# Performance work log

Hardware: AMD Instinct MI355X
Metric: run time of the kernel (lower is better)

Reference implementation:

```python
import jax, jax.numpy as jnp
import numpy as np

N = 50000          # nodes
E = 1600000        # edges
F_IN = 128         # node_features
H = 256            # hidden_dim
A = 16             # action_dim
G = 64             # num graphs in batch


def _sage_conv(x, src, dst, Wl, bl, Wr, num_nodes):
    # PyG SAGEConv (aggr='mean'): out = lin_l(mean_{j in N(i)} x_j) + lin_r(x_i)
    msgs = x[src]                                              # [E, F] gather
    agg = jax.ops.segment_sum(msgs, dst, num_segments=num_nodes)
    cnt = jax.ops.segment_sum(jnp.ones((src.shape[0], 1), x.dtype), dst,
                              num_segments=num_nodes)
    mean = agg / jnp.maximum(cnt, 1.0)                         # [N, F]
    return mean @ Wl + bl + x @ Wr


def setup_inputs() -> dict:
    key = jax.random.key(0)
    ks = jax.random.split(key, 16)
    s = lambda k, sh: jax.random.normal(k, sh, dtype=jnp.float32) * (1.0 / np.sqrt(sh[0]))
    inp = {
        "x": jax.random.normal(ks[0], (N, F_IN), dtype=jnp.float32),
        "edge_index": jax.random.randint(ks[1], (2, E), 0, N, dtype=jnp.int32),
        "batch": jnp.sort(jax.random.randint(ks[2], (N,), 0, G, dtype=jnp.int32)),
        # SAGEConv 1
        "Wl1": s(ks[3], (F_IN, H)), "bl1": jnp.zeros((H,), jnp.float32), "Wr1": s(ks[4], (F_IN, H)),
        # SAGEConv 2
        "Wl2": s(ks[5], (H, H)), "bl2": jnp.zeros((H,), jnp.float32), "Wr2": s(ks[6], (H, H)),
        # actor MLP
        "Wa1": s(ks[7], (H, H)), "ba1": jnp.zeros((H,), jnp.float32),
        "Wa2": s(ks[8], (H, A)), "ba2": jnp.zeros((A,), jnp.float32),
        # critic MLP
        "Wc1": s(ks[9], (H, H)), "bc1": jnp.zeros((H,), jnp.float32),
        "Wc2": s(ks[10], (H, 1)), "bc2": jnp.zeros((1,), jnp.float32),
    }
    return inp


def reference(x, edge_index, batch, Wl1, bl1, Wr1, Wl2, bl2, Wr2,
              Wa1, ba1, Wa2, ba2, Wc1, bc1, Wc2, bc2):
    src, dst = edge_index[0], edge_index[1]
    h = jax.nn.relu(_sage_conv(x, src, dst, Wl1, bl1, Wr1, N))
    h = jax.nn.relu(_sage_conv(h, src, dst, Wl2, bl2, Wr2, N))
    # global_mean_pool over graph ids
    pooled = jax.ops.segment_sum(h, batch, num_segments=G)
    gcnt = jax.ops.segment_sum(jnp.ones((N, 1), h.dtype), batch, num_segments=G)
    g = pooled / jnp.maximum(gcnt, 1.0)                        # [G, H]
    mu = jax.nn.relu(g @ Wa1 + ba1) @ Wa2 + ba2                # [G, A]
    value = jax.nn.relu(g @ Wc1 + bc1) @ Wc2 + bc2             # [G, 1]
    return mu, value
```

## Files before the change

### kernel.cpp

```cpp
#include <hip/hip_runtime.h>
#include <hip/hip_bf16.h>
#include <hip/hip_fp8.h>

#define NN 50000
#define NE 1600000
#define FIN 128
#define HH 256
#define GG 64
#define AA 16
#define NB ((NN + 255) / 256)
#define NRANGE 8
#define RSZ (NN / NRANGE)

typedef __attribute__((ext_vector_type(8))) short short8;
typedef __attribute__((ext_vector_type(4))) float f32x4;
typedef __attribute__((ext_vector_type(4))) int   i32x4;
typedef __attribute__((ext_vector_type(4))) uint  u32x4;

static __device__ __forceinline__ ushort f2b(float f) {
    union { __hip_bfloat16 h; ushort u; } v; v.h = __float2bfloat16(f); return v.u;
}
static __device__ __forceinline__ float b2f_lo(uint a) {
    union { float f; uint u; } v; v.u = a << 16; return v.f;
}
template<int SEL>
static __device__ __forceinline__ float f8tof(uint u) {
#if __has_builtin(__builtin_amdgcn_cvt_f32_fp8)
    return __builtin_amdgcn_cvt_f32_fp8(u, SEL);
#else
    union { unsigned char c; __hip_fp8_e4m3 f; } v;
    v.c = (u >> (SEL * 8)) & 0xFF;
    return (float)v.f;
#endif
}
static __device__ __forceinline__ unsigned char ftof8(float f) {
    __hip_fp8_e4m3 v(f);
    return *reinterpret_cast<unsigned char*>(&v);
}

__global__ void k_prep(const float* __restrict__ x, ushort* __restrict__ xb,
                       unsigned char* __restrict__ xf8,
                       const float* __restrict__ Wl1, const float* __restrict__ Wr1,
                       ushort* __restrict__ Wt1,
                       const float* __restrict__ Wl2, const float* __restrict__ Wr2,
                       ushort* __restrict__ Wt2,
                       int* __restrict__ degi, float* __restrict__ gz) {
    int b = blockIdx.x, t = threadIdx.x;
    if (b < 6250) {
        int i = b * 256 + t;
        float4 v = reinterpret_cast<const float4*>(x)[i];
        ushort4 o; o.x = f2b(v.x); o.y = f2b(v.y); o.z = f2b(v.z); o.w = f2b(v.w);
        reinterpret_cast<ushort4*>(xb)[i] = o;
        uchar4 p; p.x = ftof8(v.x); p.y = ftof8(v.y); p.z = ftof8(v.z); p.w = ftof8(v.w);
        reinterpret_cast<uchar4*>(xf8)[i] = p;
    } else if (b < 6506) {
        int i = (b - 6250) * 256 + t;
        int n = i / 256, k = i % 256;
        float v = (k < 128) ? Wl1[k * HH + n] : Wr1[(k - 128) * HH + n];
        Wt1[i] = f2b(v);
    } else if (b < 7018) {
        int i = (b - 6506) * 256 + t;
        int n = i / 512, k = i % 512;
        float v = (k < 256) ? Wl2[k * HH + n] : Wr2[(k - 256) * HH + n];
        Wt2[i] = f2b(v);
    } else if (b < 7214) {
        int i = (b - 7018) * 256 + t;
        if (i < NN) degi[i] = 0;
    } else {
        int i = (b - 7214) * 256 + t;
        if (i < GG + GG * HH) gz[i] = 0.0f;
    }
}

__global__ void k_degi(const int* __restrict__ dst, int* __restrict__ degi) {
    int range = blockIdx.x & 7;
    int i = (blockIdx.x >> 3) * 256 + threadIdx.x;
    if (i >= NE / 4) return;
    i32x4 d = __builtin_nontemporal_load(reinterpret_cast<const i32x4*>(dst) + i);
    int lo = range * RSZ, hi = lo + RSZ;
    if (d.x >= lo && d.x < hi) atomicAdd(&degi[d.x], 1);
    if (d.y >= lo && d.y < hi) atomicAdd(&degi[d.y], 1);
    if (d.z >= lo && d.z < hi) atomicAdd(&degi[d.z], 1);
    if (d.w >= lo && d.w < hi) atomicAdd(&degi[d.w], 1);
}

__global__ void k_gdeg(const int* __restrict__ batch, float* __restrict__ gcnt) {
    __shared__ float h[GG];
    int t = threadIdx.x;
    if (t < GG) h[t] = 0.0f;
    __syncthreads();
    int i = blockIdx.x * 256 + t;
    if (i < NN) atomicAdd(&h[batch[i]], 1.0f);
    __syncthreads();
    if (t < GG && h[t] != 0.0f) atomicAdd(&gcnt[t], h[t]);
}

__global__ void k_scan1(const int* __restrict__ degi, int* __restrict__ blocksum) {
    __shared__ int s[256];
    int t = threadIdx.x, i = blockIdx.x * 256 + t;
    s[t] = i < NN ? degi[i] : 0;
    __syncthreads();
    for (int d = 128; d > 0; d >>= 1) { if (t < d) s[t] += s[t + d]; __syncthreads(); }
    if (t == 0) blocksum[blockIdx.x] = s[0];
}

__global__ void k_scan2(const int* __restrict__ blocksum, int* __restrict__ blockoff) {
    __shared__ int s[256];
    int t = threadIdx.x;
    int v = t < NB ? blocksum[t] : 0;
    s[t] = v; __syncthreads();
    for (int d = 1; d < 256; d <<= 1) {
        int x = t >= d ? s[t - d] : 0; __syncthreads();
        s[t] += x; __syncthreads();
    }
    if (t < NB) blockoff[t] = s[t] - v;
}

__global__ void k_scan3(const int* __restrict__ degi, const int* __restrict__ blockoff,
                        int* __restrict__ offsets, int* __restrict__ cursor) {
    __shared__ int s[256];
    int t = threadIdx.x, i = blockIdx.x * 256 + t;
    int v = i < NN ? degi[i] : 0;
    s[t] = v; __syncthreads();
    for (int d = 1; d < 256; d <<= 1) {
        int x = t >= d ? s[t - d] : 0; __syncthreads();
        s[t] += x; __syncthreads();
    }
    if (i < NN) {
        int off = blockoff[blockIdx.x] + s[t] - v;
        offsets[i] = off;
        cursor[i]  = off;
    }
    if (i == 0) offsets[NN] = NE;
}

__global__ void k_fill(const int* __restrict__ src, const int* __restrict__ dst,
                       int* __restrict__ cursor, int* __restrict__ csr_src) {
    int range = blockIdx.x & 7;
    int i = (blockIdx.x >> 3) * 256 + threadIdx.x;
    if (i >= NE / 4) return;
    i32x4 d = __builtin_nontemporal_load(reinterpret_cast<const i32x4*>(dst) + i);
    i32x4 s = __builtin_nontemporal_load(reinterpret_cast<const i32x4*>(src) + i);
    int lo = range * RSZ, hi = lo + RSZ;
    if (d.x >= lo && d.x < hi) csr_src[atomicAdd(&cursor[d.x], 1)] = s.x;
    if (d.y >= lo && d.y < hi) csr_src[atomicAdd(&cursor[d.y], 1)] = s.y;
    if (d.z >= lo && d.z < hi) csr_src[atomicAdd(&cursor[d.z], 1)] = s.z;
    if (d.w >= lo && d.w < hi) csr_src[atomicAdd(&cursor[d.w], 1)] = s.w;
}

template<int C>
__global__ void __launch_bounds__(256) k_gatherf8(
        const int* __restrict__ offsets, const int* __restrict__ csr_src,
        const unsigned char* __restrict__ feat, ushort* __restrict__ agg) {
    constexpr int V = C / 64;
    int wid = threadIdx.x >> 6, lane = threadIdx.x & 63;
    int node = blockIdx.x * 4 + wid;
    if (node >= NN) return;
    int o0 = offsets[node], o1 = offsets[node + 1];
    const unsigned char* fp = feat + lane * V;
    float acc[V];
#pragma unroll
    for (int i = 0; i < V; i++) acc[i] = 0.0f;

    int t = o0;
    for (; t + 3 < o1; t += 4) {
        int s0 = __builtin_nontemporal_load(csr_src + t);
        int s1 = __builtin_nontemporal_load(csr_src + t + 1);
        int s2 = __builtin_nontemporal_load(csr_src + t + 2);
        int s3 = __builtin_nontemporal_load(csr_src + t + 3);
        if constexpr (V == 2) {
            uint u0 = *(const ushort*)(fp + (size_t)s0 * C);
            uint u1 = *(const ushort*)(fp + (size_t)s1 * C);
            uint u2 = *(const ushort*)(fp + (size_t)s2 * C);
            uint u3 = *(const ushort*)(fp + (size_t)s3 * C);
            acc[0] += (f8tof<0>(u0) + f8tof<0>(u1)) + (f8tof<0>(u2) + f8tof<0>(u3));
            acc[1] += (f8tof<1>(u0) + f8tof<1>(u1)) + (f8tof<1>(u2) + f8tof<1>(u3));
        } else {
            uint u0 = *(const uint*)(fp + (size_t)s0 * C);
            uint u1 = *(const uint*)(fp + (size_t)s1 * C);
            uint u2 = *(const uint*)(fp + (size_t)s2 * C);
            uint u3 = *(const uint*)(fp + (size_t)s3 * C);
            acc[0] += (f8tof<0>(u0) + f8tof<0>(u1)) + (f8tof<0>(u2) + f8tof<0>(u3));
            acc[1] += (f8tof<1>(u0) + f8tof<1>(u1)) + (f8tof<1>(u2) + f8tof<1>(u3));
            acc[2] += (f8tof<2>(u0) + f8tof<2>(u1)) + (f8tof<2>(u2) + f8tof<2>(u3));
            acc[3] += (f8tof<3>(u0) + f8tof<3>(u1)) + (f8tof<3>(u2) + f8tof<3>(u3));
        }
    }
    for (; t < o1; ++t) {
        int s0 = __builtin_nontemporal_load(csr_src + t);
        if constexpr (V == 2) {
            uint u0 = *(const ushort*)(fp + (size_t)s0 * C);
            acc[0] += f8tof<0>(u0); acc[1] += f8tof<1>(u0);
        } else {
            uint u0 = *(const uint*)(fp + (size_t)s0 * C);
            acc[0] += f8tof<0>(u0); acc[1] += f8tof<1>(u0);
            acc[2] += f8tof<2>(u0); acc[3] += f8tof<3>(u0);
        }
    }

    int deg = o1 - o0;
    float r = __builtin_amdgcn_rcpf(deg > 1 ? (float)deg : 1.0f);
    if constexpr (V == 2) {
        uint o = (uint)f2b(acc[0] * r) | ((uint)f2b(acc[1] * r) << 16);
        *(uint*)(agg + (size_t)node * C + lane * 2) = o;
    } else {
        uint2 o;
        o.x = (uint)f2b(acc[0] * r) | ((uint)f2b(acc[1] * r) << 16);
        o.y = (uint)f2b(acc[2] * r) | ((uint)f2b(acc[3] * r) << 16);
        *(uint2*)(agg + (size_t)node * C + lane * 4) = o;
    }
}

template<int K>
__global__ void __launch_bounds__(256) k_sage_mfma(
        const ushort* __restrict__ agg, const ushort* __restrict__ xin,
        const ushort* __restrict__ Wt, const float* __restrict__ bias,
        ushort* __restrict__ outb, unsigned char* __restrict__ out8) {
    constexpr int KH = K / 2;
    constexpr int LDP = 40;
    __shared__ ushort As[128 * LDP];
    __shared__ ushort Bs[256 * LDP];

    const int tid  = threadIdx.x;
    const int lane = tid & 63;
    const int w    = tid >> 6;
    const int base = blockIdx.x * 128;
    const int r    = lane & 15;
    const int kh   = lane >> 4;
    const int wcol = w * 64;

    f32x4 acc[8][4];
#pragma unroll
    for (int m = 0; m < 8; m++)
#pragma unroll
        for (int n = 0; n < 4; n++) acc[m][n] = (f32x4){0.f, 0.f, 0.f, 0.f};

    const int frowA = tid >> 1;
    const int fqA   = tid & 1;
    const int frowB = tid >> 2;
    const int fqB   = tid & 3;
    int fnode = base + frowA; if (fnode >= NN) fnode = 0;

    for (int k0 = 0; k0 < K; k0 += 32) {
        __syncthreads();
        {
            const ushort* srcp = (k0 < KH)
                ? agg + (size_t)fnode * KH + k0 + fqA * 16
                : xin + (size_t)fnode * KH + (k0 - KH) + fqA * 16;
            u32x4 a0 = *(const u32x4*)srcp;
            u32x4 a1 = *(const u32x4*)(srcp + 8);
            *(u32x4*)(&As[frowA * LDP + fqA * 16])     = a0;
            *(u32x4*)(&As[frowA * LDP + fqA * 16 + 8]) = a1;
        }
#pragma unroll
        for (int s = 0; s < 4; s++) {
            int c = frowB + s * 64;
            *(u32x4*)(&Bs[c * LDP + fqB * 8]) =
                *(const u32x4*)(Wt + (size_t)c * K + k0 + fqB * 8);
        }
        __syncthreads();

        short8 av[8], bv[4];
#pragma unroll
        for (int m = 0; m < 8; m++)
            av[m] = *(const short8*)(&As[(m * 16 + r) * LDP + kh * 8]);
#pragma unroll
        for (int n = 0; n < 4; n++)
            bv[n] = *(const short8*)(&Bs[(wcol + n * 16 + r) * LDP + kh * 8]);
#pragma unroll
        for (int m = 0; m < 8; m++)
#pragma unroll
            for (int n = 0; n < 4; n++)
                acc[m][n] = __builtin_amdgcn_mfma_f32_16x16x32_bf16(
                    av[m], bv[n], acc[m][n], 0, 0, 0);
    }

    float bj[4];
#pragma unroll
    for (int n = 0; n < 4; n++) bj[n] = bias[wcol + n * 16 + r];

#pragma unroll
    for (int m = 0; m < 8; m++) {
        int rowbase = base + m * 16 + (lane >> 4) * 4;
#pragma unroll
        for (int reg = 0; reg < 4; reg++) {
            int nd = rowbase + reg;
            if (nd < NN) {
#pragma unroll
                for (int n = 0; n < 4; n++) {
                    float v = acc[m][n][reg] + bj[n];
                    v = v > 0.0f ? v : 0.0f;
                    outb[(size_t)nd * HH + wcol + n * 16 + r] = f2b(v);
                    if (out8) out8[(size_t)nd * HH + wcol + n * 16 + r] = ftof8(v);
                }
            }
        }
    }
}

__global__ void k_pool(const ushort* __restrict__ h, const int* __restrict__ batch,
                       float* __restrict__ gpool) {
    __shared__ int sb[32];
    int j = threadIdx.x;
    int base = blockIdx.x * 32;
    int n = NN - base; if (n > 32) n = 32;
    if (j < n) sb[j] = batch[base + j];
    __syncthreads();
    float acc = 0.0f;
    int cur = sb[0];
    for (int t = 0; t < n; t++) {
        int g = sb[t];
        if (g != cur) {
            atomicAdd(&gpool[cur * HH + j], acc);
            acc = 0.0f;
            cur = g;
        }
        acc += b2f_lo((uint)h[(size_t)(base + t) * HH + j]);
    }
    atomicAdd(&gpool[cur * HH + j], acc);
}

__global__ void k_head(const float* __restrict__ gpool, const float* __restrict__ gcnt,
                       const float* __restrict__ Wa1, const float* __restrict__ ba1,
                       const float* __restrict__ Wa2, const float* __restrict__ ba2,
                       const float* __restrict__ Wc1, const float* __restrict__ bc1,
                       const float* __restrict__ Wc2, const float* __restrict__ bc2,
                       float* __restrict__ outp) {
    __shared__ float gv[HH], ha[HH], hc[HH];
    int g = blockIdx.x, j = threadIdx.x;
    float c = gcnt[g];
    c = c > 1.0f ? c : 1.0f;
    gv[j] = gpool[g * HH + j] * __builtin_amdgcn_rcpf(c);
    __syncthreads();
    float a_acc = ba1[j], c_acc = bc1[j];
#pragma unroll 2
    for (int k = 0; k < HH; k += 4) {
        float4 g4 = *reinterpret_cast<const float4*>(&gv[k]);
        const float* WA = Wa1 + k * HH + j;
        const float* WC = Wc1 + k * HH + j;
        a_acc += g4.x * WA[0] + g4.y * WA[HH] + g4.z * WA[2 * HH] + g4.w * WA[3 * HH];
        c_acc += g4.x * WC[0] + g4.y * WC[HH] + g4.z * WC[2 * HH] + g4.w * WC[3 * HH];
    }
    ha[j] = a_acc > 0.0f ? a_acc : 0.0f;
    hc[j] = c_acc > 0.0f ? c_acc : 0.0f;
    __syncthreads();
    if (j < AA) {
        float m = ba2[j];
        for (int k = 0; k < HH; k++) m += ha[k] * Wa2[k * AA + j];
        outp[g * AA + j] = m;
    } else if (j == AA) {
        float v = bc2[0];
        for (int k = 0; k < HH; k++) v += hc[k] * Wc2[k];
        outp[GG * AA + g] = v;
    }
}

extern "C" void kernel_launch(void* const* d_in, const int* in_sizes, int n_in,
                              void* d_out, int out_size, void* d_ws, size_t ws_size,
                              hipStream_t stream) {
    const float* x     = (const float*)d_in[0];
    const int*   ei    = (const int*)d_in[1];
    const int*   batch = (const int*)d_in[2];
    const float* Wl1 = (const float*)d_in[3];
    const float* bl1 = (const float*)d_in[4];
    const float* Wr1 = (const float*)d_in[5];
    const float* Wl2 = (const float*)d_in[6];
    const float* bl2 = (const float*)d_in[7];
    const float* Wr2 = (const float*)d_in[8];
    const float* Wa1 = (const float*)d_in[9];
    const float* ba1 = (const float*)d_in[10];
    const float* Wa2 = (const float*)d_in[11];
    const float* ba2 = (const float*)d_in[12];
    const float* Wc1 = (const float*)d_in[13];
    const float* bc1 = (const float*)d_in[14];
    const float* Wc2 = (const float*)d_in[15];
    const float* bc2 = (const float*)d_in[16];
    float* out = (float*)d_out;

    const int* srcv = ei;
    const int* dstv = ei + NE;

    char* ws = (char*)d_ws;
    int*    degi     = (int*)(ws + 0);
    int*    offsets  = (int*)(ws + 200192);
    int*    cursor   = (int*)(ws + 400640);
    int*    blocksum = (int*)(ws + 600832);
    int*    blockoff = (int*)(ws + 601856);
    float*  gcnt     = (float*)(ws + 602880);
    float*  gpool    = (float*)(ws + 603136);
    int*    csr_src  = (int*)(ws + 668672);
    ushort* xb       = (ushort*)(ws + 7068672);
    ushort* agg1b    = (ushort*)(ws + 19868672);
    ushort* h1b      = (ushort*)(ws + 32668672);
    ushort* agg2b    = (ushort*)(ws + 58268672);
    ushort* Wt1      = (ushort*)(ws + 83868672);
    ushort* Wt2      = (ushort*)(ws + 83999744);
    unsigned char* xf8  = (unsigned char*)(ws + 84261888);
    unsigned char* h1f8 = (unsigned char*)(ws + 90661888);

    k_prep<<<7279, 256, 0, stream>>>(x, xb, xf8, Wl1, Wr1, Wt1, Wl2, Wr2, Wt2,
                                     degi, gcnt);

    const int nch = (NE / 4 + 255) / 256;
    k_degi<<<nch * NRANGE, 256, 0, stream>>>(dstv, degi);
    k_gdeg<<<(NN + 255) / 256, 256, 0, stream>>>(batch, gcnt);
    k_scan1<<<NB, 256, 0, stream>>>(degi, blocksum);
    k_scan2<<<1, 256, 0, stream>>>(blocksum, blockoff);
    k_scan3<<<NB, 256, 0, stream>>>(degi, blockoff, offsets, cursor);
    k_fill<<<nch * NRANGE, 256, 0, stream>>>(srcv, dstv, cursor, csr_src);

    k_gatherf8<FIN><<<(NN + 3) / 4, 256, 0, stream>>>(offsets, csr_src, xf8, agg1b);
    k_sage_mfma<2 * FIN><<<(NN + 127) / 128, 256, 0, stream>>>(agg1b, xb, Wt1, bl1, h1b, h1f8);

    k_gatherf8<HH><<<(NN + 3) / 4, 256, 0, stream>>>(offsets, csr_src, h1f8, agg2b);
    k_sage_mfma<2 * HH><<<(NN + 127) / 128, 256, 0, stream>>>(agg2b, h1b, Wt2, bl2, agg2b, nullptr);

    k_pool<<<(NN + 31) / 32, 256, 0, stream>>>(agg2b, batch, gpool);
    k_head<<<GG, 256, 0, stream>>>(gpool, gcnt, Wa1, ba1, Wa2, ba2, Wc1, bc1, Wc2, bc2, out);
}
```

Baseline: 438.6 us.

## Partition gather feature columns across XCDs so each L2 caches one slice

The fp8 neighbor-gather kernels are rewritten so that each XCD, chosen by blockIdx mod 8, handles one 64-byte column slice of the feature table for a subset of nodes. Each 16-lane subgroup processes one node's slice. The aim is to shrink the per-XCD working set of the randomly gathered feature rows so it fits in that XCD's L2, cutting HBM and cross-die traffic. In exchange, CSR indices and offsets are reread once per slice. The FIN launch also oversizes the grid, so half its blocks exit immediately. The scheme relies on the hardware's round-robin assignment of blocks to XCDs.

```diff
diff --git a/kernel.cpp b/kernel.cpp
--- a/kernel.cpp
+++ b/kernel.cpp
@@ -149,66 +149,54 @@
 }
 
 template<int C>
-__global__ void __launch_bounds__(256) k_gatherf8(
+__global__ void __launch_bounds__(256) k_gather_xcd(
         const int* __restrict__ offsets, const int* __restrict__ csr_src,
         const unsigned char* __restrict__ feat, ushort* __restrict__ agg) {
-    constexpr int V = C / 64;
-    int wid = threadIdx.x >> 6, lane = threadIdx.x & 63;
-    int node = blockIdx.x * 4 + wid;
-    if (node >= NN) return;
-    int o0 = offsets[node], o1 = offsets[node + 1];
-    const unsigned char* fp = feat + lane * V;
-    float acc[V];
-#pragma unroll
-    for (int i = 0; i < V; i++) acc[i] = 0.0f;
-
+    constexpr int NSLICE = C / 64;
+    constexpr int XPS    = 8 / NSLICE;
+    constexpr int NPS    = NN / XPS;
+    const int xcd   = blockIdx.x & 7;
+    const int chunk = blockIdx.x >> 3;
+    int slice, sub;
+    if constexpr (NSLICE == 4) { slice = xcd >> 1; sub = xcd & 1; }
+    else                       { slice = xcd >> 2; sub = xcd & 3; }
+    const int sg = threadIdx.x >> 4;
+    const int ln = threadIdx.x & 15;
+    const int loc = chunk * 16 + sg;
+    if (loc >= NPS) return;
+    const int node = sub * NPS + loc;
+    const int o0 = offsets[node], o1 = offsets[node + 1];
+    const unsigned char* fp = feat + slice * 64 + ln * 4;
+
+    float a0 = 0.f, a1 = 0.f, a2 = 0.f, a3 = 0.f;
     int t = o0;
     for (; t + 3 < o1; t += 4) {
         int s0 = __builtin_nontemporal_load(csr_src + t);
         int s1 = __builtin_nontemporal_load(csr_src + t + 1);
         int s2 = __builtin_nontemporal_load(csr_src + t + 2);
         int s3 = __builtin_nontemporal_load(csr_src + t + 3);
-        if constexpr (V == 2) {
-            uint u0 = *(const ushort*)(fp + (size_t)s0 * C);
-            uint u1 = *(const ushort*)(fp + (size_t)s1 * C);
-            uint u2 = *(const ushort*)(fp + (size_t)s2 * C);
-            uint u3 = *(const ushort*)(fp + (size_t)s3 * C);
-            acc[0] += (f8tof<0>(u0) + f8tof<0>(u1)) + (f8tof<0>(u2) + f8tof<0>(u3));
-            acc[1] += (f8tof<1>(u0) + f8tof<1>(u1)) + (f8tof<1>(u2) + f8tof<1>(u3));
-        } else {
-            uint u0 = *(const uint*)(fp + (size_t)s0 * C);
-            uint u1 = *(const uint*)(fp + (size_t)s1 * C);
-            uint u2 = *(const uint*)(fp + (size_t)s2 * C);
-            uint u3 = *(const uint*)(fp + (size_t)s3 * C);
-            acc[0] += (f8tof<0>(u0) + f8tof<0>(u1)) + (f8tof<0>(u2) + f8tof<0>(u3));
-            acc[1] += (f8tof<1>(u0) + f8tof<1>(u1)) + (f8tof<1>(u2) + f8tof<1>(u3));
-            acc[2] += (f8tof<2>(u0) + f8tof<2>(u1)) + (f8tof<2>(u2) + f8tof<2>(u3));
-            acc[3] += (f8tof<3>(u0) + f8tof<3>(u1)) + (f8tof<3>(u2) + f8tof<3>(u3));
-        }
+        uint u0 = *(const uint*)(fp + (size_t)s0 * C);
+        uint u1 = *(const uint*)(fp + (size_t)s1 * C);
+        uint u2 = *(const uint*)(fp + (size_t)s2 * C);
+        uint u3 = *(const uint*)(fp + (size_t)s3 * C);
+        a0 += (f8tof<0>(u0) + f8tof<0>(u1)) + (f8tof<0>(u2) + f8tof<0>(u3));
+        a1 += (f8tof<1>(u0) + f8tof<1>(u1)) + (f8tof<1>(u2) + f8tof<1>(u3));
+        a2 += (f8tof<2>(u0) + f8tof<2>(u1)) + (f8tof<2>(u2) + f8tof<2>(u3));
+        a3 += (f8tof<3>(u0) + f8tof<3>(u1)) + (f8tof<3>(u2) + f8tof<3>(u3));
     }
     for (; t < o1; ++t) {
         int s0 = __builtin_nontemporal_load(csr_src + t);
-        if constexpr (V == 2) {
-            uint u0 = *(const ushort*)(fp + (size_t)s0 * C);
-            acc[0] += f8tof<0>(u0); acc[1] += f8tof<1>(u0);
-        } else {
-            uint u0 = *(const uint*)(fp + (size_t)s0 * C);
-            acc[0] += f8tof<0>(u0); acc[1] += f8tof<1>(u0);
-            acc[2] += f8tof<2>(u0); acc[3] += f8tof<3>(u0);
-        }
+        uint u0 = *(const uint*)(fp + (size_t)s0 * C);
+        a0 += f8tof<0>(u0); a1 += f8tof<1>(u0);
+        a2 += f8tof<2>(u0); a3 += f8tof<3>(u0);
     }
 
     int deg = o1 - o0;
     float r = __builtin_amdgcn_rcpf(deg > 1 ? (float)deg : 1.0f);
-    if constexpr (V == 2) {
-        uint o = (uint)f2b(acc[0] * r) | ((uint)f2b(acc[1] * r) << 16);
-        *(uint*)(agg + (size_t)node * C + lane * 2) = o;
-    } else {
-        uint2 o;
-        o.x = (uint)f2b(acc[0] * r) | ((uint)f2b(acc[1] * r) << 16);
-        o.y = (uint)f2b(acc[2] * r) | ((uint)f2b(acc[3] * r) << 16);
-        *(uint2*)(agg + (size_t)node * C + lane * 4) = o;
-    }
+    uint2 o;
+    o.x = (uint)f2b(a0 * r) | ((uint)f2b(a1 * r) << 16);
+    o.y = (uint)f2b(a2 * r) | ((uint)f2b(a3 * r) << 16);
+    *(uint2*)(agg + (size_t)node * C + slice * 64 + ln * 4) = o;
 }
 
 template<int K>
@@ -409,10 +397,16 @@
     k_scan3<<<NB, 256, 0, stream>>>(degi, blockoff, offsets, cursor);
     k_fill<<<nch * NRANGE, 256, 0, stream>>>(srcv, dstv, cursor, csr_src);
 
-    k_gatherf8<FIN><<<(NN + 3) / 4, 256, 0, stream>>>(offsets, csr_src, xf8, agg1b);
+    {
+        const int npb = ((NN / 2) + 15) / 16;
+        k_gather_xcd<FIN><<<npb * 8, 256, 0, stream>>>(offsets, csr_src, xf8, agg1b);
+    }
     k_sage_mfma<2 * FIN><<<(NN + 127) / 128, 256, 0, stream>>>(agg1b, xb, Wt1, bl1, h1b, h1f8);
 
-    k_gatherf8<HH><<<(NN + 3) / 4, 256, 0, stream>>>(offsets, csr_src, h1f8, agg2b);
+    {
+        const int npb = ((NN / 2) + 15) / 16;
+        k_gather_xcd<HH><<<npb * 8, 256, 0, stream>>>(offsets, csr_src, h1f8, agg2b);
+    }
     k_sage_mfma<2 * HH><<<(NN + 127) / 128, 256, 0, stream>>>(agg2b, h1b, Wt2, bl2, agg2b, nullptr);
 
     k_pool<<<(NN + 31) / 32, 256, 0, stream>>>(agg2b, batch, gpool);
```

Measured after the change: 465.4 us. +6.1%, slower.
